# Kernel tuning notes

Hardware: AMD Instinct MI355X
Metric: run time of the kernel (lower is better)

## Reference

```python
import jax, jax.numpy as jnp
import numpy as np

TAU = 0.2
EPS = 1e-12  # matches torch F.normalize eps


def setup_inputs() -> dict:
    key = jax.random.key(0)
    k1, k2 = jax.random.split(key)
    N, D = 8192, 128
    h1 = jax.random.normal(k1, (N, D), dtype=jnp.float32)
    h2 = jax.random.normal(k2, (N, D), dtype=jnp.float32)
    return {"h1": h1, "h2": h2}


def _l2norm(x):
    # torch.nn.functional.normalize: x / max(||x||, eps)
    n = jnp.sqrt(jnp.sum(x * x, axis=1, keepdims=True))
    return x / jnp.maximum(n, EPS)


def _nt_xent(h1, h2):
    h1n = _l2norm(h1)
    h2n = _l2norm(h2)
    inter = jnp.exp((h1n @ h1n.T) / TAU)  # [N, N]
    intra = jnp.exp((h1n @ h2n.T) / TAU)  # [N, N]
    pos = jnp.diagonal(intra)
    neg = inter.sum(axis=1) + intra.sum(axis=1) - jnp.diagonal(inter)
    return -jnp.log(pos / neg)  # [N]


def reference(h1, h2):
    l1 = _nt_xent(h1, h2)
    l2 = _nt_xent(h2, h1)
    return jnp.mean((l1 + l2) * 0.5)
```

## Files before the change

### kernel.cpp

```cpp
#include <hip/hip_runtime.h>
#include <math.h>


constexpr int D = 128;
constexpr float E5 = 148.4131591025766f;
constexpr int NSLOT = 81;

typedef __attribute__((ext_vector_type(16))) float f32x16;
typedef __attribute__((ext_vector_type(8)))  int   v8i;
typedef __attribute__((ext_vector_type(4)))  long  v4l;

__global__ __launch_bounds__(256) void normalize_kernel(
    const float2* __restrict__ h1, const float2* __restrict__ h2,
    unsigned short* __restrict__ P16, float* __restrict__ d12,
    float* __restrict__ out, int N)
{
    const float SC = sqrtf(5.0f * 1.44269504088896340736f);
    if (blockIdx.x * 256 + threadIdx.x == 0) out[0] = 0.f;

    int row  = blockIdx.x * 4 + (threadIdx.x >> 6);
    int lane = threadIdx.x & 63;
    float2 u = h1[(size_t)row * 64 + lane];
    float2 w = h2[(size_t)row * 64 + lane];
    float ss1 = u.x * u.x + u.y * u.y;
    float ss2 = w.x * w.x + w.y * w.y;
    float s12 = u.x * w.x + u.y * w.y;
#pragma unroll
    for (int off = 32; off > 0; off >>= 1) {
        ss1 += __shfl_xor(ss1, off, 64);
        ss2 += __shfl_xor(ss2, off, 64);
        s12 += __shfl_xor(s12, off, 64);
    }
    float n1 = fmaxf(sqrtf(ss1), 1e-12f);
    float n2 = fmaxf(sqrtf(ss2), 1e-12f);
    float c1 = SC / n1, c2 = SC / n2;
    int p1 = __builtin_amdgcn_cvt_pk_fp8_f32(u.x * c1, u.y * c1, 0, false);
    int p2 = __builtin_amdgcn_cvt_pk_fp8_f32(w.x * c2, w.y * c2, 0, false);
    int r1 = row, r2 = N + row;
    int fi = lane >> 2, li = lane & 3;
    P16[(size_t)(((r1 >> 5) * 16 + fi) * 128) + (r1 & 31) * 4 + li] =
        (unsigned short)(p1 & 0xffff);
    P16[(size_t)(((r2 >> 5) * 16 + fi) * 128) + (r2 & 31) * 4 + li] =
        (unsigned short)(p2 & 0xffff);
    if (lane == 0) d12[row] = 5.f * s12 / (n1 * n2);
}

__device__ __forceinline__ v8i load_op(const unsigned char* p) {
    v4l t;
    t[0] = *(const long*)(p);
    t[1] = *(const long*)(p + 256);
    t[2] = *(const long*)(p + 512);
    t[3] = *(const long*)(p + 768);
    return __builtin_bit_cast(v8i, t);
}

__global__ __launch_bounds__(256, 2) void gram_mfma_kernel(
    const unsigned char* __restrict__ P, float* __restrict__ part, int N)
{
    const int I = blockIdx.x;
    int nT = 4, dBase = 0;
    if (blockIdx.y < 16) { dBase = blockIdx.y * 4; }
    else if (I < 64)     { nT = 1; dBase = 64; }
    else return;

    __shared__ float ldsRow[128];
    __shared__ float ldsCol[4][128];

    const int tx   = threadIdx.x;
    const int lane = tx & 63;
    const int l32  = lane & 31, lhi = lane >> 5;
    const int wi   = (tx >> 6) >> 1, wj = (tx >> 6) & 1;
    const int iBase = I * 128;
    const int fOff = lhi * 1024;

    if (tx < 128) ldsRow[tx] = 0.f;
    {
        float* lc = &ldsCol[0][0];
        lc[tx] = 0.f;
        lc[tx + 256] = 0.f;
    }
    __syncthreads();

    v8i a[2][2];
#pragma unroll
    for (int st = 0; st < 2; ++st) {
        const unsigned char* xp =
            P + (size_t)(I * 4 + wi * 2 + st) * 4096 + fOff + l32 * 8;
#pragma unroll
        for (int kc = 0; kc < 2; ++kc)
            a[st][kc] = load_op(xp + kc * 2048);
    }

    float racc0[16], racc1[16];
#pragma unroll
    for (int r = 0; r < 16; ++r) { racc0[r] = 0.f; racc1[r] = 0.f; }

    const int j0 = wj * 64 + l32;
    const int j1 = j0 + 32;

#pragma unroll
    for (int t = 0; t < 4; ++t) {
        if (t >= nT) break;

        const int J = (I + dBase + t) & 127;
        const unsigned char* pb =
            P + (size_t)(J * 4 + wj * 2) * 4096 + fOff + l32 * 8;

        v8i b0[2], b1[2];
#pragma unroll
        for (int kc = 0; kc < 2; ++kc) {
            b0[kc] = load_op(pb + kc * 2048);
            b1[kc] = load_op(pb + 4096 + kc * 2048);
        }

        f32x16 acc00, acc01, acc10, acc11;
#pragma unroll
        for (int r = 0; r < 16; ++r) {
            acc00[r] = 0.f; acc01[r] = 0.f; acc10[r] = 0.f; acc11[r] = 0.f;
        }

#pragma unroll
        for (int kc = 0; kc < 2; ++kc) {
            acc00 = __builtin_amdgcn_mfma_scale_f32_32x32x64_f8f6f4(
                a[0][kc], b0[kc], acc00, 0, 0, 0, 127, 0, 127);
            acc10 = __builtin_amdgcn_mfma_scale_f32_32x32x64_f8f6f4(
                a[1][kc], b0[kc], acc10, 0, 0, 0, 127, 0, 127);
            acc01 = __builtin_amdgcn_mfma_scale_f32_32x32x64_f8f6f4(
                a[0][kc], b1[kc], acc01, 0, 0, 0, 127, 0, 127);
            acc11 = __builtin_amdgcn_mfma_scale_f32_32x32x64_f8f6f4(
                a[1][kc], b1[kc], acc11, 0, 0, 0, 127, 0, 127);
        }

        float c0 = 0.f, c1 = 0.f;
#pragma unroll
        for (int r = 0; r < 16; ++r) {
            float e00 = __builtin_amdgcn_exp2f(acc00[r]);
            float e01 = __builtin_amdgcn_exp2f(acc01[r]);
            float e10 = __builtin_amdgcn_exp2f(acc10[r]);
            float e11 = __builtin_amdgcn_exp2f(acc11[r]);
            racc0[r] += e00 + e01;
            racc1[r] += e10 + e11;
            c0 += e00 + e10;
            c1 += e01 + e11;
        }
        if ((dBase + t) != 0) {
            c0 += __shfl_xor(c0, 32, 64);
            c1 += __shfl_xor(c1, 32, 64);
            if (lane < 32) {
                atomicAdd(&ldsCol[t][j0], c0);
                atomicAdd(&ldsCol[t][j1], c1);
            }
        }
    }

#pragma unroll
    for (int r = 0; r < 16; ++r) {
        float s0 = racc0[r], s1 = racc1[r];
#pragma unroll
        for (int off = 1; off < 32; off <<= 1) {
            s0 += __shfl_xor(s0, off, 64);
            s1 += __shfl_xor(s1, off, 64);
        }
        if (l32 == 0) {
            int rowm = (r & 3) + 8 * (r >> 2) + 4 * lhi;
            atomicAdd(&ldsRow[wi * 64 + rowm], s0);
            atomicAdd(&ldsRow[wi * 64 + 32 + rowm], s1);
        }
    }

    __syncthreads();

    if (tx < 128) {
        const int y = blockIdx.y;
        part[(size_t)y * (2 * N) + iBase + tx] = ldsRow[tx];
#pragma unroll
        for (int t = 0; t < 4; ++t) {
            if (t >= nT) break;
            const int J = (I + dBase + t) & 127;
            const size_t slot = (y < 16) ? (size_t)(17 + y * 4 + t) : 16;
            part[slot * (2 * N) + (size_t)J * 128 + tx] = ldsCol[t][tx];
        }
    }
}

__global__ __launch_bounds__(256) void loss_reduce_kernel(
    const float* __restrict__ part, const float* __restrict__ d12,
    float* __restrict__ out, int N)
{
    __shared__ float sm[256];
    float s = 0.f;
    for (int i = blockIdx.x * 256 + threadIdx.x; i < N; i += gridDim.x * 256) {
        float r1 = 0.f, r2 = 0.f;
#pragma unroll 9
        for (int sl = 0; sl < NSLOT; ++sl) {
            r1 += part[(size_t)sl * (2 * N) + i];
            r2 += part[(size_t)sl * (2 * N) + N + i];
        }
        s += 0.5f * (logf(r1 - E5) + logf(r2 - E5)) - d12[i];
    }
    sm[threadIdx.x] = s;
    __syncthreads();
    for (int w = 128; w > 0; w >>= 1) {
        if (threadIdx.x < w) sm[threadIdx.x] += sm[threadIdx.x + w];
        __syncthreads();
    }
    if (threadIdx.x == 0) atomicAdd(out, sm[0] / (float)N);
}

extern "C" void kernel_launch(void* const* d_in, const int* in_sizes, int n_in,
                              void* d_out, int out_size, void* d_ws, size_t ws_size,
                              hipStream_t stream) {
    const float* h1 = (const float*)d_in[0];
    const float* h2 = (const float*)d_in[1];
    const int N = in_sizes[0] / D;

    unsigned char* P = (unsigned char*)d_ws;
    float* part = (float*)(P + (size_t)2 * N * D);
    float* d12  = part + (size_t)NSLOT * 2 * N;
    float* out  = (float*)d_out;

    normalize_kernel<<<N / 4, 256, 0, stream>>>(
        (const float2*)h1, (const float2*)h2,
        (unsigned short*)P, d12, out, N);

    dim3 grid(128, 17, 1);
    gram_mfma_kernel<<<grid, 256, 0, stream>>>(P, part, N);

    loss_reduce_kernel<<<32, 256, 0, stream>>>(part, d12, out, N);
}
```

Measured before the change: 119.3 us.

## Widen normalize stores, split gram tile across 8 waves, enlarge reduce grid

The normalize kernel now handles 32 rows per block with float4 loads, packs four fp8 values per convert, and writes 8-byte chunks directly into the tiled operand layout instead of scattered 2-byte stores. The gram kernel goes from 4 to 8 waves per block, each computing a 32x64 subtile with half the accumulators and A-operand registers, to raise occupancy and latency hiding. The cost is that B operands are loaded redundantly by more waves and there is more LDS atomic contention. The loss reduction grid is doubled.

```diff
diff --git a/kernel.cpp b/kernel.cpp
--- a/kernel.cpp
+++ b/kernel.cpp
@@ -11,22 +11,33 @@
 typedef __attribute__((ext_vector_type(4)))  long  v4l;
 
 __global__ __launch_bounds__(256) void normalize_kernel(
-    const float2* __restrict__ h1, const float2* __restrict__ h2,
-    unsigned short* __restrict__ P16, float* __restrict__ d12,
+    const float4* __restrict__ h1, const float4* __restrict__ h2,
+    unsigned char* __restrict__ P, float* __restrict__ d12,
     float* __restrict__ out, int N)
 {
     const float SC = sqrtf(5.0f * 1.44269504088896340736f);
-    if (blockIdx.x * 256 + threadIdx.x == 0) out[0] = 0.f;
-
-    int row  = blockIdx.x * 4 + (threadIdx.x >> 6);
-    int lane = threadIdx.x & 63;
-    float2 u = h1[(size_t)row * 64 + lane];
-    float2 w = h2[(size_t)row * 64 + lane];
-    float ss1 = u.x * u.x + u.y * u.y;
-    float ss2 = w.x * w.x + w.y * w.y;
-    float s12 = u.x * w.x + u.y * w.y;
-#pragma unroll
-    for (int off = 32; off > 0; off >>= 1) {
+    if (blockIdx.x == 0 && threadIdx.x == 0) out[0] = 0.f;
+
+    const int tx   = threadIdx.x;
+    const int rloc = tx >> 3;
+    const int t    = tx & 7;
+    const int row  = blockIdx.x * 32 + rloc;
+
+    float4 u[4], w[4];
+#pragma unroll
+    for (int i = 0; i < 4; ++i) {
+        u[i] = h1[(size_t)row * 32 + t * 4 + i];
+        w[i] = h2[(size_t)row * 32 + t * 4 + i];
+    }
+    float ss1 = 0.f, ss2 = 0.f, s12 = 0.f;
+#pragma unroll
+    for (int i = 0; i < 4; ++i) {
+        ss1 += u[i].x*u[i].x + u[i].y*u[i].y + u[i].z*u[i].z + u[i].w*u[i].w;
+        ss2 += w[i].x*w[i].x + w[i].y*w[i].y + w[i].z*w[i].z + w[i].w*w[i].w;
+        s12 += u[i].x*w[i].x + u[i].y*w[i].y + u[i].z*w[i].z + u[i].w*w[i].w;
+    }
+#pragma unroll
+    for (int off = 4; off > 0; off >>= 1) {
         ss1 += __shfl_xor(ss1, off, 64);
         ss2 += __shfl_xor(ss2, off, 64);
         s12 += __shfl_xor(s12, off, 64);
@@ -34,15 +45,36 @@
     float n1 = fmaxf(sqrtf(ss1), 1e-12f);
     float n2 = fmaxf(sqrtf(ss2), 1e-12f);
     float c1 = SC / n1, c2 = SC / n2;
-    int p1 = __builtin_amdgcn_cvt_pk_fp8_f32(u.x * c1, u.y * c1, 0, false);
-    int p2 = __builtin_amdgcn_cvt_pk_fp8_f32(w.x * c2, w.y * c2, 0, false);
-    int r1 = row, r2 = N + row;
-    int fi = lane >> 2, li = lane & 3;
-    P16[(size_t)(((r1 >> 5) * 16 + fi) * 128) + (r1 & 31) * 4 + li] =
-        (unsigned short)(p1 & 0xffff);
-    P16[(size_t)(((r2 >> 5) * 16 + fi) * 128) + (r2 & 31) * 4 + li] =
-        (unsigned short)(p2 & 0xffff);
-    if (lane == 0) d12[row] = 5.f * s12 / (n1 * n2);
+    if (t == 0) d12[row] = 5.f * s12 / (n1 * n2);
+
+    int u0 = __builtin_amdgcn_cvt_pk_fp8_f32(u[0].x*c1, u[0].y*c1, 0, false);
+    u0     = __builtin_amdgcn_cvt_pk_fp8_f32(u[0].z*c1, u[0].w*c1, u0, true);
+    int u1 = __builtin_amdgcn_cvt_pk_fp8_f32(u[1].x*c1, u[1].y*c1, 0, false);
+    u1     = __builtin_amdgcn_cvt_pk_fp8_f32(u[1].z*c1, u[1].w*c1, u1, true);
+    int u2 = __builtin_amdgcn_cvt_pk_fp8_f32(u[2].x*c1, u[2].y*c1, 0, false);
+    u2     = __builtin_amdgcn_cvt_pk_fp8_f32(u[2].z*c1, u[2].w*c1, u2, true);
+    int u3 = __builtin_amdgcn_cvt_pk_fp8_f32(u[3].x*c1, u[3].y*c1, 0, false);
+    u3     = __builtin_amdgcn_cvt_pk_fp8_f32(u[3].z*c1, u[3].w*c1, u3, true);
+    int w0 = __builtin_amdgcn_cvt_pk_fp8_f32(w[0].x*c2, w[0].y*c2, 0, false);
+    w0     = __builtin_amdgcn_cvt_pk_fp8_f32(w[0].z*c2, w[0].w*c2, w0, true);
+    int w1 = __builtin_amdgcn_cvt_pk_fp8_f32(w[1].x*c2, w[1].y*c2, 0, false);
+    w1     = __builtin_amdgcn_cvt_pk_fp8_f32(w[1].z*c2, w[1].w*c2, w1, true);
+    int w2 = __builtin_amdgcn_cvt_pk_fp8_f32(w[2].x*c2, w[2].y*c2, 0, false);
+    w2     = __builtin_amdgcn_cvt_pk_fp8_f32(w[2].z*c2, w[2].w*c2, w2, true);
+    int w3 = __builtin_amdgcn_cvt_pk_fp8_f32(w[3].x*c2, w[3].y*c2, 0, false);
+    w3     = __builtin_amdgcn_cvt_pk_fp8_f32(w[3].z*c2, w[3].w*c2, w3, true);
+
+    unsigned long long ulo = (unsigned)u0 | ((unsigned long long)(unsigned)u1 << 32);
+    unsigned long long uhi = (unsigned)u2 | ((unsigned long long)(unsigned)u3 << 32);
+    unsigned long long wlo = (unsigned)w0 | ((unsigned long long)(unsigned)w1 << 32);
+    unsigned long long whi = (unsigned)w2 | ((unsigned long long)(unsigned)w3 << 32);
+
+    size_t b1 = (size_t)blockIdx.x * 4096 + (size_t)t * 512 + (size_t)rloc * 8;
+    size_t b2 = ((size_t)(N >> 5) + blockIdx.x) * 4096 + (size_t)t * 512 + (size_t)rloc * 8;
+    *(unsigned long long*)(P + b1)       = ulo;
+    *(unsigned long long*)(P + b1 + 256) = uhi;
+    *(unsigned long long*)(P + b2)       = wlo;
+    *(unsigned long long*)(P + b2 + 256) = whi;
 }
 
 __device__ __forceinline__ v8i load_op(const unsigned char* p) {
@@ -54,7 +86,7 @@
     return __builtin_bit_cast(v8i, t);
 }
 
-__global__ __launch_bounds__(256, 2) void gram_mfma_kernel(
+__global__ __launch_bounds__(512, 4) void gram_mfma_kernel(
     const unsigned char* __restrict__ P, float* __restrict__ part, int N)
 {
     const int I = blockIdx.x;
@@ -69,34 +101,29 @@
     const int tx   = threadIdx.x;
     const int lane = tx & 63;
     const int l32  = lane & 31, lhi = lane >> 5;
-    const int wi   = (tx >> 6) >> 1, wj = (tx >> 6) & 1;
+    const int wid  = tx >> 6;
+    const int wr   = wid >> 1;
+    const int wc   = wid & 1;
     const int iBase = I * 128;
     const int fOff = lhi * 1024;
 
     if (tx < 128) ldsRow[tx] = 0.f;
+    ((float*)ldsCol)[tx] = 0.f;
+    __syncthreads();
+
+    v8i a[2];
     {
-        float* lc = &ldsCol[0][0];
-        lc[tx] = 0.f;
-        lc[tx + 256] = 0.f;
-    }
-    __syncthreads();
-
-    v8i a[2][2];
-#pragma unroll
-    for (int st = 0; st < 2; ++st) {
         const unsigned char* xp =
-            P + (size_t)(I * 4 + wi * 2 + st) * 4096 + fOff + l32 * 8;
-#pragma unroll
-        for (int kc = 0; kc < 2; ++kc)
-            a[st][kc] = load_op(xp + kc * 2048);
-    }
-
-    float racc0[16], racc1[16];
-#pragma unroll
-    for (int r = 0; r < 16; ++r) { racc0[r] = 0.f; racc1[r] = 0.f; }
-
-    const int j0 = wj * 64 + l32;
-    const int j1 = j0 + 32;
+            P + (size_t)(I * 4 + wr) * 4096 + fOff + l32 * 8;
+        a[0] = load_op(xp);
+        a[1] = load_op(xp + 2048);
+    }
+
+    float racc[16];
+#pragma unroll
+    for (int r = 0; r < 16; ++r) racc[r] = 0.f;
+
+    const int j0 = wc * 64 + l32;
 
 #pragma unroll
     for (int t = 0; t < 4; ++t) {
@@ -104,7 +131,7 @@
 
         const int J = (I + dBase + t) & 127;
         const unsigned char* pb =
-            P + (size_t)(J * 4 + wj * 2) * 4096 + fOff + l32 * 8;
+            P + (size_t)(J * 4 + wc * 2) * 4096 + fOff + l32 * 8;
 
         v8i b0[2], b1[2];
 #pragma unroll
@@ -113,58 +140,46 @@
             b1[kc] = load_op(pb + 4096 + kc * 2048);
         }
 
-        f32x16 acc00, acc01, acc10, acc11;
+        f32x16 acc0, acc1;
+#pragma unroll
+        for (int r = 0; r < 16; ++r) { acc0[r] = 0.f; acc1[r] = 0.f; }
+
+#pragma unroll
+        for (int kc = 0; kc < 2; ++kc) {
+            acc0 = __builtin_amdgcn_mfma_scale_f32_32x32x64_f8f6f4(
+                a[kc], b0[kc], acc0, 0, 0, 0, 127, 0, 127);
+            acc1 = __builtin_amdgcn_mfma_scale_f32_32x32x64_f8f6f4(
+                a[kc], b1[kc], acc1, 0, 0, 0, 127, 0, 127);
+        }
+
+        float c0 = 0.f, c1 = 0.f;
 #pragma unroll
         for (int r = 0; r < 16; ++r) {
-            acc00[r] = 0.f; acc01[r] = 0.f; acc10[r] = 0.f; acc11[r] = 0.f;
-        }
-
-#pragma unroll
-        for (int kc = 0; kc < 2; ++kc) {
-            acc00 = __builtin_amdgcn_mfma_scale_f32_32x32x64_f8f6f4(
-                a[0][kc], b0[kc], acc00, 0, 0, 0, 127, 0, 127);
-            acc10 = __builtin_amdgcn_mfma_scale_f32_32x32x64_f8f6f4(
-                a[1][kc], b0[kc], acc10, 0, 0, 0, 127, 0, 127);
-            acc01 = __builtin_amdgcn_mfma_scale_f32_32x32x64_f8f6f4(
-                a[0][kc], b1[kc], acc01, 0, 0, 0, 127, 0, 127);
-            acc11 = __builtin_amdgcn_mfma_scale_f32_32x32x64_f8f6f4(
-                a[1][kc], b1[kc], acc11, 0, 0, 0, 127, 0, 127);
-        }
-
-        float c0 = 0.f, c1 = 0.f;
-#pragma unroll
-        for (int r = 0; r < 16; ++r) {
-            float e00 = __builtin_amdgcn_exp2f(acc00[r]);
-            float e01 = __builtin_amdgcn_exp2f(acc01[r]);
-            float e10 = __builtin_amdgcn_exp2f(acc10[r]);
-            float e11 = __builtin_amdgcn_exp2f(acc11[r]);
-            racc0[r] += e00 + e01;
-            racc1[r] += e10 + e11;
-            c0 += e00 + e10;
-            c1 += e01 + e11;
+            float e0 = __builtin_amdgcn_exp2f(acc0[r]);
+            float e1 = __builtin_amdgcn_exp2f(acc1[r]);
+            racc[r] += e0 + e1;
+            c0 += e0;
+            c1 += e1;
         }
         if ((dBase + t) != 0) {
             c0 += __shfl_xor(c0, 32, 64);
             c1 += __shfl_xor(c1, 32, 64);
             if (lane < 32) {
                 atomicAdd(&ldsCol[t][j0], c0);
-                atomicAdd(&ldsCol[t][j1], c1);
+                atomicAdd(&ldsCol[t][j0 + 32], c1);
             }
         }
     }
 
 #pragma unroll
     for (int r = 0; r < 16; ++r) {
-        float s0 = racc0[r], s1 = racc1[r];
-#pragma unroll
-        for (int off = 1; off < 32; off <<= 1) {
-            s0 += __shfl_xor(s0, off, 64);
-            s1 += __shfl_xor(s1, off, 64);
-        }
+        float s = racc[r];
+#pragma unroll
+        for (int off = 1; off < 32; off <<= 1)
+            s += __shfl_xor(s, off, 64);
         if (l32 == 0) {
             int rowm = (r & 3) + 8 * (r >> 2) + 4 * lhi;
-            atomicAdd(&ldsRow[wi * 64 + rowm], s0);
-            atomicAdd(&ldsRow[wi * 64 + 32 + rowm], s1);
+            atomicAdd(&ldsRow[wr * 32 + rowm], s);
         }
     }
 
@@ -219,12 +234,11 @@
     float* d12  = part + (size_t)NSLOT * 2 * N;
     float* out  = (float*)d_out;
 
-    normalize_kernel<<<N / 4, 256, 0, stream>>>(
-        (const float2*)h1, (const float2*)h2,
-        (unsigned short*)P, d12, out, N);
+    normalize_kernel<<<N / 32, 256, 0, stream>>>(
+        (const float4*)h1, (const float4*)h2, P, d12, out, N);
 
     dim3 grid(128, 17, 1);
-    gram_mfma_kernel<<<grid, 256, 0, stream>>>(P, part, N);
-
-    loss_reduce_kernel<<<32, 256, 0, stream>>>(part, d12, out, N);
-}
+    gram_mfma_kernel<<<grid, 512, 0, stream>>>(P, part, N);
+
+    loss_reduce_kernel<<<64, 256, 0, stream>>>(part, d12, out, N);
+}
```

After: 138.8 us. +16.3%, slower.
